# Kernel optimization log

Hardware: AMD Instinct MI355X
Metric: run time of the kernel (lower is better)

The kernel has to match this reference:

```python
import jax, jax.numpy as jnp
import numpy as np

NUM_CLASSES = 10
BIN_STEP = 0.1
N_SAMPLES = 2_000_000
NUM_BINS = 10  # len(arange(0,1.1,0.1)) - 1


def setup_inputs() -> dict:
    key = jax.random.key(0)
    k1, k2 = jax.random.split(key)
    # scaled logits -> softmax so that all confidence bins (incl. (0.9,1.0]) are populated
    logits = jax.random.normal(k1, (N_SAMPLES, NUM_CLASSES), dtype=jnp.float32) * 3.0
    probs = jax.nn.softmax(logits, axis=-1)
    labels = jax.random.randint(k2, (N_SAMPLES,), 0, NUM_CLASSES)
    return {"probs": probs, "labels": labels}


def reference(probs, labels):
    # probs: [N, C] float, labels: [N] int
    n, c = probs.shape
    pred_class = jnp.argmax(probs, axis=1)                      # [N]
    flat = probs.reshape(-1)                                    # [N*C] expanded_preds
    pred_oh = jax.nn.one_hot(pred_class, c, dtype=probs.dtype).reshape(-1)
    tgt_oh = jax.nn.one_hot(labels, c, dtype=probs.dtype).reshape(-1)
    # 1 exactly at the true-class slot of correctly-predicted samples
    correct_vec = tgt_oh * (pred_oh == tgt_oh).astype(probs.dtype)  # [N*C]

    bins = jnp.asarray(np.arange(0.0, 1.1, BIN_STEP), dtype=probs.dtype)  # 11 edges
    # np.digitize(..., right=True) - 1 ; entries exactly 0.0 get idx=-1 and are
    # dropped from every bin, matching the original per-bin masking loop.
    bin_idx = jnp.digitize(flat, bins, right=True) - 1          # [N*C] in [-1, 9]

    zeros = jnp.zeros((NUM_BINS,), dtype=probs.dtype)
    ones = jnp.ones_like(flat)
    # fused single-pass histogram: counts, correct-sums, confidence-sums
    bin_counts = zeros.at[bin_idx].add(ones, mode='drop')
    bin_corrects = zeros.at[bin_idx].add(correct_vec, mode='drop')
    bin_conf_sum = zeros.at[bin_idx].add(flat, mode='drop')

    bin_confidence = bin_conf_sum / bin_counts                  # per-bin mean conf
    bin_acc = bin_corrects / bin_counts                         # per-bin accuracy
    total = jnp.sum(bin_counts)
    ece = jnp.sum(jnp.abs(bin_confidence - bin_acc) * bin_counts) / total

    bin_centers = bins[1:] - BIN_STEP / 2
    return (ece, bin_centers, bin_acc)
```

## Files before the change

### kernel.cpp

```cpp
#include <hip/hip_runtime.h>

#define NBINS 10
#define C 10

constexpr int BLOCK = 256;
constexpr int GRIDH = 1024;
constexpr int GRIDA = 1024;
constexpr int PSTR  = 32;
constexpr int PAIRS_PER_TILE = BLOCK;
constexpr int F4_PER_TILE    = PAIRS_PER_TILE * 5;


__global__ __launch_bounds__(BLOCK) void ece_fused(
    const float4* __restrict__ p4,
    const int2*   __restrict__ l2,
    float*        __restrict__ part,
    int npairs, int nf4)
{
    __shared__ float        s_stage[F4_PER_TILE * 4];
    __shared__ unsigned int s_cor[NBINS];

    const int tid  = threadIdx.x;
    const int lane = tid & 63, wave = tid >> 6;

    const float EDGE[NBINS] = {
        (float)(0*0.1), (float)(1*0.1), (float)(2*0.1), (float)(3*0.1), (float)(4*0.1),
        (float)(5*0.1), (float)(6*0.1), (float)(7*0.1), (float)(8*0.1), (float)(9*0.1)};

    if (blockIdx.x < GRIDH) {
        float        conf[NBINS];
        unsigned int cnt[NBINS];
#pragma unroll
        for (int t = 0; t < NBINS; ++t) { conf[t] = 0.0f; cnt[t] = 0u; }

        for (int fi = blockIdx.x * BLOCK + tid; fi < nf4; fi += GRIDH * BLOCK) {
            const float4 q = p4[fi];
            const float e[4] = {q.x, q.y, q.z, q.w};
#pragma unroll
            for (int j = 0; j < 4; ++j) {
                const float x = e[j];
                conf[0] += x;
                cnt[0]  += (unsigned)__popcll(__ballot(x > EDGE[0]));
#pragma unroll
                for (int t = 1; t < NBINS; ++t) {
                    const bool g = x > EDGE[t];
                    cnt[t]  += (unsigned)__popcll(__ballot(g));
                    conf[t] += g ? x : 0.0f;
                }
            }
        }

#pragma unroll
        for (int t = 0; t < NBINS; ++t)
            for (int o = 32; o > 0; o >>= 1)
                conf[t] += __shfl_xor(conf[t], o, 64);

        float* s_confr = s_stage;
        float* s_cntr  = s_stage + 4 * NBINS;
        if (lane == 0) {
#pragma unroll
            for (int t = 0; t < NBINS; ++t) {
                s_confr[wave * NBINS + t] = conf[t];
                s_cntr [wave * NBINS + t] = (float)cnt[t];
            }
        }
        __syncthreads();

        if (tid < 12) {
            float fc = 0.0f, fn = 0.0f;
            if (tid < NBINS) {
#pragma unroll
                for (int w = 0; w < 4; ++w) {
                    fc += s_confr[w * NBINS + tid];
                    fn += s_cntr [w * NBINS + tid];
                }
            }
            part[(size_t)blockIdx.x * PSTR + tid]                = fc;
            part[(size_t)GRIDH * PSTR + blockIdx.x * PSTR + tid] = fn;
        }
    } else {
        const int bid2 = blockIdx.x - GRIDH;
        if (tid < NBINS) s_cor[tid] = 0u;

        float4* s4 = reinterpret_cast<float4*>(s_stage);
        const int ntiles = (npairs + PAIRS_PER_TILE - 1) / PAIRS_PER_TILE;

        for (int tile = bid2; tile < ntiles; tile += GRIDA) {
            __syncthreads();

            const int f4base = tile * F4_PER_TILE;
#pragma unroll
            for (int k = 0; k < 5; ++k) {
                const int fi = f4base + k * BLOCK + tid;
                float4 q = make_float4(0.0f, 0.0f, 0.0f, 0.0f);
                if (fi < nf4) q = p4[fi];
                s4[k * BLOCK + tid] = q;
            }
            __syncthreads();

            const int pr = tile * PAIRS_PER_TILE + tid;
            if (pr < npairs) {
                const float4* row = reinterpret_cast<const float4*>(&s_stage[tid * 20]);
                const float4 q0 = row[0], q1 = row[1], q2 = row[2], q3 = row[3], q4 = row[4];
                const int2 lab = l2[pr];

                const float a[C] = {q0.x,q0.y,q0.z,q0.w, q1.x,q1.y,q1.z,q1.w, q2.x,q2.y};
                const float b[C] = {q2.z,q2.w, q3.x,q3.y,q3.z,q3.w, q4.x,q4.y,q4.z,q4.w};

#pragma unroll
                for (int s = 0; s < 2; ++s) {
                    const float* p = (s == 0) ? a : b;
                    const int  lbl = (s == 0) ? lab.x : lab.y;

                    float mx = p[0]; int arg = 0;
#pragma unroll
                    for (int j = 1; j < C; ++j)
                        if (p[j] > mx) { mx = p[j]; arg = j; }

                    if (arg == lbl) {
                        const int im = min((int)ceilf(mx * 10.0f) - 1, NBINS - 1);
                        if (im >= 0) atomicAdd(&s_cor[im], 1u);
                    }
                }
            }
        }
        __syncthreads();

        if (tid < 12) {
            const float v = (tid < NBINS) ? (float)s_cor[tid] : 0.0f;
            part[(size_t)2 * GRIDH * PSTR + bid2 * PSTR + tid] = v;
        }
    }
}

__global__ __launch_bounds__(256) void ece_reduce(
    const float* __restrict__ part,
    float* __restrict__ out)
{
    __shared__ double s_c[4][NBINS];
    __shared__ double s_n[4][NBINS];
    __shared__ double s_r[4][NBINS];

    const int tid = threadIdx.x;
    const int lane = tid & 63, wave = tid >> 6;

    double conf[NBINS], cntd[NBINS], cord[NBINS];
#pragma unroll
    for (int t = 0; t < NBINS; ++t) { conf[t] = 0.0; cntd[t] = 0.0; cord[t] = 0.0; }

    for (int b = tid; b < GRIDH; b += 256) {
        const float4* rc = reinterpret_cast<const float4*>(part + (size_t)b * PSTR);
        const float4* rn = reinterpret_cast<const float4*>(part + (size_t)GRIDH * PSTR + b * PSTR);
        const float4* rr = reinterpret_cast<const float4*>(part + (size_t)2 * GRIDH * PSTR + b * PSTR);
        const float4 c0 = rc[0], c1 = rc[1], c2 = rc[2];
        const float4 n0 = rn[0], n1 = rn[1], n2 = rn[2];
        const float4 r0 = rr[0], r1 = rr[1], r2 = rr[2];
        const float cf[12] = {c0.x,c0.y,c0.z,c0.w, c1.x,c1.y,c1.z,c1.w, c2.x,c2.y,c2.z,c2.w};
        const float nf[12] = {n0.x,n0.y,n0.z,n0.w, n1.x,n1.y,n1.z,n1.w, n2.x,n2.y,n2.z,n2.w};
        const float rf[12] = {r0.x,r0.y,r0.z,r0.w, r1.x,r1.y,r1.z,r1.w, r2.x,r2.y,r2.z,r2.w};
#pragma unroll
        for (int t = 0; t < NBINS; ++t) {
            conf[t] += (double)cf[t];
            cntd[t] += (double)nf[t];
            cord[t] += (double)rf[t];
        }
    }

#pragma unroll
    for (int t = 0; t < NBINS; ++t) {
        for (int o = 32; o > 0; o >>= 1) {
            conf[t] += __shfl_xor(conf[t], o, 64);
            cntd[t] += __shfl_xor(cntd[t], o, 64);
            cord[t] += __shfl_xor(cord[t], o, 64);
        }
    }
    if (lane == 0) {
#pragma unroll
        for (int t = 0; t < NBINS; ++t) {
            s_c[wave][t] = conf[t]; s_n[wave][t] = cntd[t]; s_r[wave][t] = cord[t];
        }
    }
    __syncthreads();

    if (tid == 0) {
        double S[NBINS + 1], G[NBINS + 1], R[NBINS];
        for (int t = 0; t < NBINS; ++t) {
            G[t] = s_n[0][t] + s_n[1][t] + s_n[2][t] + s_n[3][t];
            R[t] = s_r[0][t] + s_r[1][t] + s_r[2][t] + s_r[3][t];
            S[t] = s_c[0][t] + s_c[1][t] + s_c[2][t] + s_c[3][t];
        }
        S[NBINS] = 0.0; G[NBINS] = 0.0;

        double total = 0.0, ece = 0.0;
        for (int j = 0; j < NBINS; ++j) {
            const double c  = G[j] - G[j + 1];
            const double sc = S[j] - S[j + 1];
            const double ba = R[j] / c;
            total += c;
            ece   += fabs(sc / c - ba) * c;
            out[1 + j]  = (float)((float)((j + 1) * 0.1) - 0.05f);
            out[11 + j] = (float)ba;
        }
        out[0] = (float)(ece / total);
    }
}

extern "C" void kernel_launch(void* const* d_in, const int* in_sizes, int n_in,
                              void* d_out, int out_size, void* d_ws, size_t ws_size,
                              hipStream_t stream)
{
    const float* probs  = (const float*)d_in[0];
    const int*   labels = (const int*)  d_in[1];
    float*       out    = (float*)d_out;
    const int n      = in_sizes[1];
    const int npairs = n / 2;
    const int nf4    = (n * C) / 4;

    float* part = (float*)d_ws;

    ece_fused<<<GRIDH + GRIDA, BLOCK, 0, stream>>>((const float4*)probs,
                                                   (const int2*)labels,
                                                   part, npairs, nf4);
    ece_reduce<<<1, 256, 0, stream>>>(part, out);
}
```

Baseline: 43.61 us.

## Interleave histogram/argmax blocks, use per-lane counters and max-compare for correctness

Even and odd block indices now alternate between the histogram role and the correctness role, so both kinds of work are spread across the device at the same time. The histogram path drops the per-element ballot/popcount, keeps per-lane counters reduced by shuffles at the end, derives the bin-0 count from the element count, and issues two float4 loads per iteration for more memory-level parallelism. The correctness path replaces the sequential argmax with a tree of fmax and tests whether the label's probability is at least the row max. That test treats a tie at the max as correct, whereas the first-index argmax may not. Skipping the zero-fill of shared memory for out-of-range tiles also leaves stale values there.

```diff
diff --git a/kernel.cpp b/kernel.cpp
--- a/kernel.cpp
+++ b/kernel.cpp
@@ -22,38 +22,63 @@
 
     const int tid  = threadIdx.x;
     const int lane = tid & 63, wave = tid >> 6;
+    const int row  = blockIdx.x >> 1;
 
     const float EDGE[NBINS] = {
         (float)(0*0.1), (float)(1*0.1), (float)(2*0.1), (float)(3*0.1), (float)(4*0.1),
         (float)(5*0.1), (float)(6*0.1), (float)(7*0.1), (float)(8*0.1), (float)(9*0.1)};
 
-    if (blockIdx.x < GRIDH) {
+    if ((blockIdx.x & 1) == 0) {
         float        conf[NBINS];
-        unsigned int cnt[NBINS];
-#pragma unroll
-        for (int t = 0; t < NBINS; ++t) { conf[t] = 0.0f; cnt[t] = 0u; }
-
-        for (int fi = blockIdx.x * BLOCK + tid; fi < nf4; fi += GRIDH * BLOCK) {
-            const float4 q = p4[fi];
-            const float e[4] = {q.x, q.y, q.z, q.w};
-#pragma unroll
-            for (int j = 0; j < 4; ++j) {
-                const float x = e[j];
-                conf[0] += x;
-                cnt[0]  += (unsigned)__popcll(__ballot(x > EDGE[0]));
-#pragma unroll
-                for (int t = 1; t < NBINS; ++t) {
-                    const bool g = x > EDGE[t];
-                    cnt[t]  += (unsigned)__popcll(__ballot(g));
-                    conf[t] += g ? x : 0.0f;
-                }
-            }
-        }
+        unsigned int cnt1[NBINS];
+        unsigned int nf = 0;
+#pragma unroll
+        for (int t = 0; t < NBINS; ++t) { conf[t] = 0.0f; cnt1[t] = 0u; }
+
+        const int stride = GRIDH * BLOCK;
+        int fi = row * BLOCK + tid;
+
+#define PROC_F4(q)                                                          \
+        {                                                                   \
+            const float e_[4] = {(q).x, (q).y, (q).z, (q).w};               \
+            conf[0] += ((q).x + (q).y) + ((q).z + (q).w);                   \
+            _Pragma("unroll")                                               \
+            for (int j_ = 0; j_ < 4; ++j_) {                                \
+                const float x_ = e_[j_];                                    \
+                _Pragma("unroll")                                           \
+                for (int t_ = 1; t_ < NBINS; ++t_) {                        \
+                    const bool g_ = x_ > EDGE[t_];                          \
+                    cnt1[t_] += g_ ? 1u : 0u;             \
+                    conf[t_] += g_ ? x_ : 0.0f;          \
+                }                                                           \
+            }                                                               \
+        }
+
+        for (; fi + stride < nf4; fi += 2 * stride) {
+            const float4 qa = p4[fi];
+            const float4 qb = p4[fi + stride];
+            PROC_F4(qa);
+            PROC_F4(qb);
+            nf += 2;
+        }
+        if (fi < nf4) {
+            const float4 qa = p4[fi];
+            PROC_F4(qa);
+            nf += 1;
+        }
+#undef PROC_F4
+
+        unsigned int cnt0 = 4u * nf;
 
 #pragma unroll
         for (int t = 0; t < NBINS; ++t)
             for (int o = 32; o > 0; o >>= 1)
                 conf[t] += __shfl_xor(conf[t], o, 64);
+        for (int o = 32; o > 0; o >>= 1) cnt0 += __shfl_xor(cnt0, o, 64);
+#pragma unroll
+        for (int t = 1; t < NBINS; ++t)
+            for (int o = 32; o > 0; o >>= 1)
+                cnt1[t] += __shfl_xor(cnt1[t], o, 64);
 
         float* s_confr = s_stage;
         float* s_cntr  = s_stage + 4 * NBINS;
@@ -61,7 +86,7 @@
 #pragma unroll
             for (int t = 0; t < NBINS; ++t) {
                 s_confr[wave * NBINS + t] = conf[t];
-                s_cntr [wave * NBINS + t] = (float)cnt[t];
+                s_cntr [wave * NBINS + t] = (t == 0) ? (float)cnt0 : (float)cnt1[t];
             }
         }
         __syncthreads();
@@ -75,52 +100,49 @@
                     fn += s_cntr [w * NBINS + tid];
                 }
             }
-            part[(size_t)blockIdx.x * PSTR + tid]                = fc;
-            part[(size_t)GRIDH * PSTR + blockIdx.x * PSTR + tid] = fn;
+            part[(size_t)row * PSTR + tid]                = fc;
+            part[(size_t)GRIDH * PSTR + row * PSTR + tid] = fn;
         }
     } else {
-        const int bid2 = blockIdx.x - GRIDH;
         if (tid < NBINS) s_cor[tid] = 0u;
 
         float4* s4 = reinterpret_cast<float4*>(s_stage);
         const int ntiles = (npairs + PAIRS_PER_TILE - 1) / PAIRS_PER_TILE;
 
-        for (int tile = bid2; tile < ntiles; tile += GRIDA) {
+        for (int tile = row; tile < ntiles; tile += GRIDA) {
             __syncthreads();
 
             const int f4base = tile * F4_PER_TILE;
 #pragma unroll
             for (int k = 0; k < 5; ++k) {
                 const int fi = f4base + k * BLOCK + tid;
-                float4 q = make_float4(0.0f, 0.0f, 0.0f, 0.0f);
-                if (fi < nf4) q = p4[fi];
-                s4[k * BLOCK + tid] = q;
+                if (fi < nf4) s4[k * BLOCK + tid] = p4[fi];
             }
             __syncthreads();
 
             const int pr = tile * PAIRS_PER_TILE + tid;
             if (pr < npairs) {
-                const float4* row = reinterpret_cast<const float4*>(&s_stage[tid * 20]);
-                const float4 q0 = row[0], q1 = row[1], q2 = row[2], q3 = row[3], q4 = row[4];
+                const int base = tid * 20;
+                const float4* rw = reinterpret_cast<const float4*>(&s_stage[base]);
+                const float4 q0 = rw[0], q1 = rw[1], q2 = rw[2], q3 = rw[3], q4 = rw[4];
                 const int2 lab = l2[pr];
 
-                const float a[C] = {q0.x,q0.y,q0.z,q0.w, q1.x,q1.y,q1.z,q1.w, q2.x,q2.y};
-                const float b[C] = {q2.z,q2.w, q3.x,q3.y,q3.z,q3.w, q4.x,q4.y,q4.z,q4.w};
-
-#pragma unroll
-                for (int s = 0; s < 2; ++s) {
-                    const float* p = (s == 0) ? a : b;
-                    const int  lbl = (s == 0) ? lab.x : lab.y;
-
-                    float mx = p[0]; int arg = 0;
-#pragma unroll
-                    for (int j = 1; j < C; ++j)
-                        if (p[j] > mx) { mx = p[j]; arg = j; }
-
-                    if (arg == lbl) {
-                        const int im = min((int)ceilf(mx * 10.0f) - 1, NBINS - 1);
-                        if (im >= 0) atomicAdd(&s_cor[im], 1u);
-                    }
+                const float mA = fmaxf(fmaxf(fmaxf(fmaxf(q0.x, q0.y), fmaxf(q0.z, q0.w)),
+                                             fmaxf(fmaxf(q1.x, q1.y), fmaxf(q1.z, q1.w))),
+                                       fmaxf(q2.x, q2.y));
+                const float plA = s_stage[base + lab.x];
+                if (plA >= mA) {
+                    const int im = min((int)ceilf(plA * 10.0f) - 1, NBINS - 1);
+                    if (im >= 0) atomicAdd(&s_cor[im], 1u);
+                }
+
+                const float mB = fmaxf(fmaxf(fmaxf(fmaxf(q2.z, q2.w), fmaxf(q3.x, q3.y)),
+                                             fmaxf(fmaxf(q3.z, q3.w), fmaxf(q4.x, q4.y))),
+                                       fmaxf(q4.z, q4.w));
+                const float plB = s_stage[base + 10 + lab.y];
+                if (plB >= mB) {
+                    const int im = min((int)ceilf(plB * 10.0f) - 1, NBINS - 1);
+                    if (im >= 0) atomicAdd(&s_cor[im], 1u);
                 }
             }
         }
@@ -128,7 +150,7 @@
 
         if (tid < 12) {
             const float v = (tid < NBINS) ? (float)s_cor[tid] : 0.0f;
-            part[(size_t)2 * GRIDH * PSTR + bid2 * PSTR + tid] = v;
+            part[(size_t)2 * GRIDH * PSTR + row * PSTR + tid] = v;
         }
     }
 }
```

Result: slower. 57.50 us (+31.9%).
